# Performance work log

Measured on AMD Instinct MI355X. Metric: run time of the kernel, lower is better.

Reference implementation:

```python
import jax, jax.numpy as jnp
import numpy as np

N = 50000      # nodes
E = 800000     # edges (avg degree 16)
D = 96         # input_size == output_size
C = 10         # n_class
STEPS = 4      # num_layers -> GGNN propagation steps


def setup_inputs() -> dict:
    key = jax.random.key(0)
    ks = jax.random.split(key, 12)
    s = 1.0 / np.sqrt(D)
    return {
        "x": jax.random.normal(ks[0], (N, D), dtype=jnp.float32),
        "src": jax.random.randint(ks[1], (E,), 0, N, dtype=jnp.int32),
        "dst": jax.random.randint(ks[2], (E,), 0, N, dtype=jnp.int32),
        # edge message transform (DGL GatedGraphConv: Linear(out, out) per etype, 1 etype)
        "W_e": jax.random.normal(ks[3], (D, D), dtype=jnp.float32) * s,
        "b_e": jax.random.normal(ks[4], (D,), dtype=jnp.float32) * s,
        # GRUCell params (torch layout: rows ordered r, z, n)
        "W_ih": jax.random.normal(ks[5], (3 * D, D), dtype=jnp.float32) * s,
        "W_hh": jax.random.normal(ks[6], (3 * D, D), dtype=jnp.float32) * s,
        "b_ih": jax.random.normal(ks[7], (3 * D,), dtype=jnp.float32) * s,
        "b_hh": jax.random.normal(ks[8], (3 * D,), dtype=jnp.float32) * s,
        # classifier head
        "W_fc": jax.random.normal(ks[9], (C, D), dtype=jnp.float32) * s,
        "b_fc": jax.random.normal(ks[10], (C,), dtype=jnp.float32) * s,
    }


def _gru_cell(a, h, W_ih, W_hh, b_ih, b_hh):
    # torch.nn.GRUCell math; gate order r, z, n
    gx = a @ W_ih.T + b_ih            # [N, 3D]
    gh = h @ W_hh.T + b_hh            # [N, 3D]
    xr, xz, xn = jnp.split(gx, 3, axis=-1)
    hr, hz, hn = jnp.split(gh, 3, axis=-1)
    r = jax.nn.sigmoid(xr + hr)
    z = jax.nn.sigmoid(xz + hz)
    n = jnp.tanh(xn + r * hn)
    return (1.0 - z) * n + z * h


def reference(x, src, dst, W_e, b_e, W_ih, W_hh, b_ih, b_hh, W_fc, b_fc):
    h = x  # in_feats == out_feats, no padding needed
    for _ in range(STEPS):
        m = h @ W_e.T + b_e                                  # per-node transform [N, D]
        a = jax.ops.segment_sum(m[src], dst, num_segments=N) # gather + scatter-add [N, D]
        h = _gru_cell(a, h, W_ih, W_hh, b_ih, b_hh)
    logits = jax.nn.elu(h) @ W_fc.T + b_fc                   # [N, C]
    return logits
```

## Files before the change

### kernel.cpp

```cpp
#include <hip/hip_runtime.h>

static constexpr int D = 96;
static constexpr int G3 = 3 * D;
static constexpr int NSTEPS = 4;
static constexpr int NT = 18;
static constexpr int SCAN_BLK = 1024;
static constexpr int SLP = 104;
static constexpr int PLS = 97;
static constexpr int PLANE = 16 * PLS;

typedef __attribute__((ext_vector_type(8))) _Float16 f16x8;
typedef __attribute__((ext_vector_type(4))) _Float16 f16x4;
typedef __attribute__((ext_vector_type(4))) float f32x4;

__device__ __forceinline__ f16x8 load_a_frag(const _Float16* __restrict__ base,
                                             int r0, int lane, int kc) {
  int row = r0 + (lane & 15);
  int k0 = kc * 32 + ((lane >> 4) << 3);
  return *(const f16x8*)(base + (size_t)row * D + k0);
}

__device__ __forceinline__ f16x8 load_b_swz(const _Float16* __restrict__ W,
                                            int t, int kc, int lane) {
  return *(const f16x8*)(W + (((size_t)t * 3 + kc) * 64 + lane) * 8);
}


__global__ void convert_x_kernel(const float* __restrict__ x,
                                 _Float16* __restrict__ h, int total4) {
  int i = blockIdx.x * blockDim.x + threadIdx.x;
  if (i >= total4) return;
  float4 v = ((const float4*)x)[i];
  f16x4 o;
  o[0] = (_Float16)v.x; o[1] = (_Float16)v.y;
  o[2] = (_Float16)v.z; o[3] = (_Float16)v.w;
  *(f16x4*)(h + (size_t)i * 4) = o;
}

__global__ void compute_wx_kernel(const float* __restrict__ Wih,
                                  const float* __restrict__ We,
                                  const float* __restrict__ be,
                                  float* __restrict__ Wx,
                                  float* __restrict__ bxe) {
  int idx = blockIdx.x * blockDim.x + threadIdx.x;
  if (idx < G3 * D) {
    int r = idx / D, k = idx - r * D;
    float acc = 0.f;
    for (int c = 0; c < D; ++c) acc += Wih[r * D + c] * We[c * D + k];
    Wx[idx] = acc;
  } else if (idx < G3 * D + G3) {
    int r = idx - G3 * D;
    float acc = 0.f;
    for (int c = 0; c < D; ++c) acc += Wih[r * D + c] * be[c];
    bxe[r] = acc;
  }
}

__global__ void swizzle_f16_kernel(const float* __restrict__ Wx,
                                   const float* __restrict__ Whh,
                                   _Float16* __restrict__ WxF,
                                   _Float16* __restrict__ WhhF) {
  int idx = blockIdx.x * blockDim.x + threadIdx.x;
  if (idx >= 2 * NT * 3 * 64) return;
  int mat = idx / (NT * 3 * 64);
  int rem = idx - mat * (NT * 3 * 64);
  int t = rem / (3 * 64);
  int rem2 = rem - t * (3 * 64);
  int kc = rem2 >> 6;
  int lane = rem2 & 63;
  int c = t * 16 + (lane & 15);
  int k0 = kc * 32 + ((lane >> 4) << 3);
  const float* W = mat ? Whh : Wx;
  _Float16* dF = mat ? WhhF : WxF;
  f16x8 o;
#pragma unroll
  for (int j = 0; j < 8; ++j) o[j] = (_Float16)W[(size_t)c * D + k0 + j];
  *(f16x8*)(dF + (((size_t)t * 3 + kc) * 64 + lane) * 8) = o;
}


__global__ void hist_kernel(const int* __restrict__ dst, int* __restrict__ counts, int E) {
  int e = blockIdx.x * blockDim.x + threadIdx.x;
  if (e < E) atomicAdd(&counts[dst[e]], 1);
}

__global__ void partial_sum_kernel(const int* __restrict__ counts,
                                   int* __restrict__ blk_sums, int n) {
  __shared__ int red[256];
  int base = blockIdx.x * SCAN_BLK;
  int tid = threadIdx.x;
  int s = 0;
#pragma unroll
  for (int j = 0; j < 4; ++j) {
    int i = base + j * 256 + tid;
    if (i < n) s += counts[i];
  }
  red[tid] = s;
  __syncthreads();
  for (int off = 128; off > 0; off >>= 1) {
    if (tid < off) red[tid] += red[tid + off];
    __syncthreads();
  }
  if (tid == 0) blk_sums[blockIdx.x] = red[0];
}

__global__ void scan_offsets_kernel(const int* __restrict__ blk_sums,
                                    int* __restrict__ blk_off,
                                    int* __restrict__ row_ptr, int nb, int n) {
  __shared__ int lds[64];
  int tid = threadIdx.x;
  if (tid < nb) lds[tid] = blk_sums[tid];
  __syncthreads();
  if (tid == 0) {
    int run = 0;
    for (int i = 0; i < nb; ++i) { blk_off[i] = run; run += lds[i]; }
    row_ptr[n] = run;
  }
}

__global__ void block_scan_kernel(const int* __restrict__ counts,
                                  const int* __restrict__ blk_off,
                                  int* __restrict__ row_ptr, int n) {
  __shared__ int red[256];
  int base = blockIdx.x * SCAN_BLK;
  int tid = threadIdx.x;
  int i0 = base + tid * 4;
  int v0 = 0, v1 = 0, v2 = 0, v3 = 0;
  if (i0 + 3 < n) {
    int4 c = *(const int4*)(counts + i0);
    v0 = c.x; v1 = c.y; v2 = c.z; v3 = c.w;
  } else {
    if (i0 < n) v0 = counts[i0];
    if (i0 + 1 < n) v1 = counts[i0 + 1];
    if (i0 + 2 < n) v2 = counts[i0 + 2];
  }
  int tsum = v0 + v1 + v2 + v3;
  red[tid] = tsum;
  __syncthreads();
  for (int off = 1; off < 256; off <<= 1) {
    int t = (tid >= off) ? red[tid - off] : 0;
    __syncthreads();
    red[tid] += t;
    __syncthreads();
  }
  int excl = blk_off[blockIdx.x] + red[tid] - tsum;
  if (i0 < n) row_ptr[i0] = excl;
  if (i0 + 1 < n) row_ptr[i0 + 1] = excl + v0;
  if (i0 + 2 < n) row_ptr[i0 + 2] = excl + v0 + v1;
  if (i0 + 3 < n) row_ptr[i0 + 3] = excl + v0 + v1 + v2;
}

__global__ void route_kernel(const int* __restrict__ src, const int* __restrict__ dst,
                             const int* __restrict__ row_ptr,
                             int* __restrict__ bucket_fill,
                             unsigned* __restrict__ stage, int E, int n) {
  __shared__ int cnt[64], gbase[64], rpb[64];
  int tid = threadIdx.x;
  int base = blockIdx.x * 1024;
  if (tid < 64) {
    cnt[tid] = 0;
    int node = tid << 10;
    rpb[tid] = row_ptr[node < n ? node : n];
  }
  __syncthreads();
  int b[4], lp[4], sv[4], dl[4];
#pragma unroll
  for (int j = 0; j < 4; ++j) {
    int e = base + tid * 4 + j;
    if (e < E) {
      sv[j] = src[e];
      int d = dst[e];
      b[j] = d >> 10;
      dl[j] = d & 1023;
      lp[j] = atomicAdd(&cnt[b[j]], 1);
    } else {
      b[j] = -1;
    }
  }
  __syncthreads();
  if (tid < 64) {
    int c = cnt[tid];
    gbase[tid] = (c > 0) ? atomicAdd(&bucket_fill[tid], c) : 0;
  }
  __syncthreads();
#pragma unroll
  for (int j = 0; j < 4; ++j) {
    if (b[j] >= 0) {
      int pos = rpb[b[j]] + gbase[b[j]] + lp[j];
      stage[pos] = (unsigned)sv[j] | ((unsigned)dl[j] << 16);
    }
  }
}

__global__ void local_fill_kernel(const unsigned* __restrict__ stage,
                                  const int* __restrict__ row_ptr,
                                  unsigned short* __restrict__ csr_src, int n) {
  __shared__ int rp[1024];
  __shared__ int lf[1024];
  int b = blockIdx.x;
  int node0 = b << 10;
  int nn = n - node0; if (nn > 1024) nn = 1024;
  int tid = threadIdx.x;
  if (tid < nn) { rp[tid] = row_ptr[node0 + tid]; lf[tid] = 0; }
  __syncthreads();
  int ebeg = row_ptr[node0];
  int eend = row_ptr[node0 + nn];
  for (int i = ebeg + tid; i < eend; i += 1024) {
    unsigned p = stage[i];
    int dl = p >> 16;
    int s = p & 0xFFFF;
    int pos = rp[dl] + atomicAdd(&lf[dl], 1);
    csr_src[pos] = (unsigned short)s;
  }
}


__device__ __forceinline__ void gru_epilogue(const float* lds,
                                             const _Float16* __restrict__ h,
                                             _Float16* __restrict__ hout,
                                             const int* __restrict__ row_ptr,
                                             const float* __restrict__ bxe,
                                             const float* __restrict__ bih,
                                             const float* __restrict__ bhh,
                                             int base_row, int tid) {
#pragma unroll
  for (int j = 0; j < 4; ++j) {
    int e = tid + j * 384;
    int row = e / D;
    int col = e - row * D;
    int grow = base_row + row;
    int a = row * PLS + col;
    float degf = (float)(row_ptr[grow + 1] - row_ptr[grow]);
    float R  = lds[a] + lds[PLANE + a];
    float Z  = lds[2 * PLANE + a] + lds[3 * PLANE + a];
    float XN = lds[4 * PLANE + a];
    float HN = lds[5 * PLANE + a];
    float rg = 1.0f / (1.0f + __expf(-(R + bih[col] + bhh[col] + degf * bxe[col])));
    float zg = 1.0f / (1.0f + __expf(-(Z + bih[D + col] + bhh[D + col] + degf * bxe[D + col])));
    float ng = tanhf(XN + bih[2 * D + col] + degf * bxe[2 * D + col] + rg * (HN + bhh[2 * D + col]));
    float hv = (float)h[(size_t)grow * D + col];
    hout[(size_t)grow * D + col] = (_Float16)((1.0f - zg) * ng + zg * hv);
  }
}

__global__ __launch_bounds__(384) void gru_fused_kernel(
    const _Float16* __restrict__ h, _Float16* __restrict__ hout,
    const int* __restrict__ row_ptr, const unsigned short* __restrict__ csr_src,
    const _Float16* __restrict__ WxF, const _Float16* __restrict__ WhhF,
    const float* __restrict__ bxe, const float* __restrict__ bih,
    const float* __restrict__ bhh, int n) {
  __shared__ float lds[6 * PLANE];
  _Float16* sl = (_Float16*)&lds[4 * PLANE];
  int r0 = blockIdx.x << 5;
  int tid = threadIdx.x;
  int w = tid >> 6;
  int lane = tid & 63;

  {
    int row = tid / 12;
    int part = tid - row * 12;
    int grow = r0 + row;
    float acc[8];
#pragma unroll
    for (int j = 0; j < 8; ++j) acc[j] = 0.f;
    if (grow < n) {
      int beg = row_ptr[grow], end = row_ptr[grow + 1];
      const _Float16* hp = h + (size_t)part * 8;
      int e = beg;
      for (; e + 7 < end; e += 8) {
        f16x8 v0 = *(const f16x8*)(hp + (size_t)csr_src[e] * D);
        f16x8 v1 = *(const f16x8*)(hp + (size_t)csr_src[e + 1] * D);
        f16x8 v2 = *(const f16x8*)(hp + (size_t)csr_src[e + 2] * D);
        f16x8 v3 = *(const f16x8*)(hp + (size_t)csr_src[e + 3] * D);
        f16x8 v4 = *(const f16x8*)(hp + (size_t)csr_src[e + 4] * D);
        f16x8 v5 = *(const f16x8*)(hp + (size_t)csr_src[e + 5] * D);
        f16x8 v6 = *(const f16x8*)(hp + (size_t)csr_src[e + 6] * D);
        f16x8 v7 = *(const f16x8*)(hp + (size_t)csr_src[e + 7] * D);
#pragma unroll
        for (int j = 0; j < 8; ++j)
          acc[j] += (((float)v0[j] + (float)v1[j]) + ((float)v2[j] + (float)v3[j])) +
                    (((float)v4[j] + (float)v5[j]) + ((float)v6[j] + (float)v7[j]));
      }
      if (e + 3 < end) {
        f16x8 v0 = *(const f16x8*)(hp + (size_t)csr_src[e] * D);
        f16x8 v1 = *(const f16x8*)(hp + (size_t)csr_src[e + 1] * D);
        f16x8 v2 = *(const f16x8*)(hp + (size_t)csr_src[e + 2] * D);
        f16x8 v3 = *(const f16x8*)(hp + (size_t)csr_src[e + 3] * D);
#pragma unroll
        for (int j = 0; j < 8; ++j)
          acc[j] += ((float)v0[j] + (float)v1[j]) + ((float)v2[j] + (float)v3[j]);
        e += 4;
      }
      for (; e < end; ++e) {
        f16x8 v = *(const f16x8*)(hp + (size_t)csr_src[e] * D);
#pragma unroll
        for (int j = 0; j < 8; ++j) acc[j] += (float)v[j];
      }
    }
    f16x8 o;
#pragma unroll
    for (int j = 0; j < 8; ++j) o[j] = (_Float16)acc[j];
    *(f16x8*)&sl[row * SLP + part * 8] = o;
  }
  __syncthreads();

  const int opS = (w < 3) ? 1 : 0;
  const _Float16* WF = opS ? WxF : WhhF;
  const int wg = opS ? w : (w - 3);
  const int t0 = wg * 6;
  const int plane = wg * 2 + (opS ? 0 : 1);

  f16x8 a0[3], a1[3];
  if (opS) {
#pragma unroll
    for (int kc = 0; kc < 3; ++kc) {
      int k0 = kc * 32 + ((lane >> 4) << 3);
      a0[kc] = *(const f16x8*)&sl[(lane & 15) * SLP + k0];
      a1[kc] = *(const f16x8*)&sl[(16 + (lane & 15)) * SLP + k0];
    }
  } else {
#pragma unroll
    for (int kc = 0; kc < 3; ++kc) {
      a0[kc] = load_a_frag(h, r0, lane, kc);
      a1[kc] = load_a_frag(h, r0 + 16, lane, kc);
    }
  }
  __syncthreads();

  f32x4 acc0[6], acc1[6];
#pragma unroll
  for (int t = 0; t < 6; ++t) {
    acc0[t] = (f32x4){0.f, 0.f, 0.f, 0.f};
    acc1[t] = (f32x4){0.f, 0.f, 0.f, 0.f};
  }

#pragma unroll
  for (int ct = 0; ct < 6; ++ct)
#pragma unroll
    for (int kc = 0; kc < 3; ++kc) {
      f16x8 b = load_b_swz(WF, t0 + ct, kc, lane);
      acc0[ct] = __builtin_amdgcn_mfma_f32_16x16x32_f16(a0[kc], b, acc0[ct], 0, 0, 0);
      acc1[ct] = __builtin_amdgcn_mfma_f32_16x16x32_f16(a1[kc], b, acc1[ct], 0, 0, 0);
    }

  int col_l = lane & 15;
  int rq = (lane >> 4) << 2;
#pragma unroll
  for (int ct = 0; ct < 6; ++ct)
#pragma unroll
    for (int q = 0; q < 4; ++q)
      lds[plane * PLANE + (rq + q) * PLS + ct * 16 + col_l] = acc0[ct][q];
  __syncthreads();
  gru_epilogue(lds, h, hout, row_ptr, bxe, bih, bhh, r0, tid);
  __syncthreads();
  if (r0 + 16 < n) {
#pragma unroll
    for (int ct = 0; ct < 6; ++ct)
#pragma unroll
      for (int q = 0; q < 4; ++q)
        lds[plane * PLANE + (rq + q) * PLS + ct * 16 + col_l] = acc1[ct][q];
    __syncthreads();
    gru_epilogue(lds, h, hout, row_ptr, bxe, bih, bhh, r0 + 16, tid);
  }
}

__global__ void head_kernel(const _Float16* __restrict__ h,
                            const float* __restrict__ Wfc,
                            const float* __restrict__ bfc,
                            float* __restrict__ out,
                            int n, int C) {
  int idx = blockIdx.x * blockDim.x + threadIdx.x;
  if (idx >= n * C) return;
  int i = idx / C;
  int c = idx - i * C;
  const _Float16* hr = h + (size_t)i * D;
  const float* wr = Wfc + (size_t)c * D;
  float acc = bfc[c];
#pragma unroll 8
  for (int k = 0; k < D; ++k) {
    float hv = (float)hr[k];
    float e = hv > 0.0f ? hv : (__expf(hv) - 1.0f);
    acc += e * wr[k];
  }
  out[idx] = acc;
}

extern "C" void kernel_launch(void* const* d_in, const int* in_sizes, int n_in,
                              void* d_out, int out_size, void* d_ws, size_t ws_size,
                              hipStream_t stream) {
  const float* x    = (const float*)d_in[0];
  const int*   src  = (const int*)d_in[1];
  const int*   dst  = (const int*)d_in[2];
  const float* W_e  = (const float*)d_in[3];
  const float* b_e  = (const float*)d_in[4];
  const float* W_ih = (const float*)d_in[5];
  const float* W_hh = (const float*)d_in[6];
  const float* b_ih = (const float*)d_in[7];
  const float* b_hh = (const float*)d_in[8];
  const float* W_fc = (const float*)d_in[9];
  const float* b_fc = (const float*)d_in[10];

  const int n = in_sizes[0] / D;
  const int E = in_sizes[1];
  const int C = out_size / n;

  _Float16* hA = (_Float16*)d_ws;
  _Float16* hB = hA + (size_t)n * D;
  float* Wx    = (float*)(hB + (size_t)n * D);
  _Float16* WxF  = (_Float16*)(Wx + (size_t)G3 * D);
  _Float16* WhhF = WxF + (size_t)G3 * D;
  float* bxe   = (float*)(WhhF + (size_t)G3 * D);
  int* counts  = (int*)(bxe + G3);
  int* bucket_fill = counts + n;
  int* row_ptr = bucket_fill + n;
  unsigned short* csr_src = (unsigned short*)(row_ptr + (n + 1));
  int* blk_sums = (int*)(csr_src + E);
  int* blk_off  = blk_sums + 64;
  unsigned* stage = (unsigned*)(blk_off + 64);

  const int threads = 256;
  const int nb = (n + SCAN_BLK - 1) / SCAN_BLK;
  const int NB = (n + 1023) >> 10;

  (void)hipMemsetAsync(counts, 0, (size_t)2 * n * sizeof(int), stream);
  hist_kernel<<<(E + threads - 1) / threads, threads, 0, stream>>>(dst, counts, E);
  partial_sum_kernel<<<nb, 256, 0, stream>>>(counts, blk_sums, n);
  scan_offsets_kernel<<<1, 64, 0, stream>>>(blk_sums, blk_off, row_ptr, nb, n);
  block_scan_kernel<<<nb, 256, 0, stream>>>(counts, blk_off, row_ptr, n);
  route_kernel<<<(E + 1023) / 1024, 256, 0, stream>>>(src, dst, row_ptr,
                                                      bucket_fill, stage, E, n);
  local_fill_kernel<<<NB, 1024, 0, stream>>>(stage, row_ptr, csr_src, n);
  compute_wx_kernel<<<(G3 * D + G3 + threads - 1) / threads, threads, 0, stream>>>(
      W_ih, W_e, b_e, Wx, bxe);
  swizzle_f16_kernel<<<(2 * NT * 3 * 64 + threads - 1) / threads, threads, 0, stream>>>(
      Wx, W_hh, WxF, WhhF);
  convert_x_kernel<<<((n * D / 4) + threads - 1) / threads, threads, 0, stream>>>(
      x, hA, n * D / 4);

  const int gridG = (n + 31) / 32;

  const _Float16* hcur = hA;
  _Float16* hnext = hB;
  for (int step = 0; step < NSTEPS; ++step) {
    gru_fused_kernel<<<gridG, 384, 0, stream>>>(hcur, hnext, row_ptr, csr_src,
                                                WxF, WhhF, bxe, b_ih, b_hh, n);
    const _Float16* t = hcur; hcur = hnext; hnext = (_Float16*)t;
  }

  const int gridH = (n * C + threads - 1) / threads;
  head_kernel<<<gridH, threads, 0, stream>>>(hcur, W_fc, b_fc, (float*)d_out, n, C);
}
```

Baseline: 342.2 us.

## Fuse weight prep kernels, fold x conversion into routing, sort CSR neighbors

Merges the Wx product and fp16 swizzle into one prep kernel that writes the swizzled fp16 weights directly, which drops the fp32 Wx intermediate and one launch. The x-to-fp16 conversion moves into route_kernel as a grid-stride loop, removing another launch. local_fill_kernel now insertion-sorts each node's source list so the gathers in the GRU kernel touch memory in a more ordered pattern. The per-node sort is serial per thread and adds preprocessing cost in exchange for better gather locality.

```diff
diff --git a/kernel.cpp b/kernel.cpp
--- a/kernel.cpp
+++ b/kernel.cpp
@@ -26,56 +26,49 @@
 }
 
 
-__global__ void convert_x_kernel(const float* __restrict__ x,
-                                 _Float16* __restrict__ h, int total4) {
-  int i = blockIdx.x * blockDim.x + threadIdx.x;
-  if (i >= total4) return;
-  float4 v = ((const float4*)x)[i];
-  f16x4 o;
-  o[0] = (_Float16)v.x; o[1] = (_Float16)v.y;
-  o[2] = (_Float16)v.z; o[3] = (_Float16)v.w;
-  *(f16x4*)(h + (size_t)i * 4) = o;
-}
-
-__global__ void compute_wx_kernel(const float* __restrict__ Wih,
-                                  const float* __restrict__ We,
-                                  const float* __restrict__ be,
-                                  float* __restrict__ Wx,
-                                  float* __restrict__ bxe) {
+__global__ void prep_weights_kernel(const float* __restrict__ Wih,
+                                    const float* __restrict__ Whh,
+                                    const float* __restrict__ We,
+                                    const float* __restrict__ be,
+                                    _Float16* __restrict__ WxF,
+                                    _Float16* __restrict__ WhhF,
+                                    float* __restrict__ bxe) {
   int idx = blockIdx.x * blockDim.x + threadIdx.x;
-  if (idx < G3 * D) {
-    int r = idx / D, k = idx - r * D;
+  const int SWZ = 2 * NT * 3 * 64;
+  if (idx < SWZ) {
+    int mat = idx / (NT * 3 * 64);
+    int rem = idx - mat * (NT * 3 * 64);
+    int t = rem / (3 * 64);
+    int rem2 = rem - t * (3 * 64);
+    int kc = rem2 >> 6;
+    int lane = rem2 & 63;
+    int c = t * 16 + (lane & 15);
+    int k0 = kc * 32 + ((lane >> 4) << 3);
+    f16x8 o;
+    if (mat == 0) {
+      float a[8] = {0.f, 0.f, 0.f, 0.f, 0.f, 0.f, 0.f, 0.f};
+      const float* wr = Wih + (size_t)c * D;
+      for (int c2 = 0; c2 < D; ++c2) {
+        float wv = wr[c2];
+        const float* werow = We + (size_t)c2 * D + k0;
+#pragma unroll
+        for (int j = 0; j < 8; ++j) a[j] += wv * werow[j];
+      }
+#pragma unroll
+      for (int j = 0; j < 8; ++j) o[j] = (_Float16)a[j];
+      *(f16x8*)(WxF + (((size_t)t * 3 + kc) * 64 + lane) * 8) = o;
+    } else {
+#pragma unroll
+      for (int j = 0; j < 8; ++j) o[j] = (_Float16)Whh[(size_t)c * D + k0 + j];
+      *(f16x8*)(WhhF + (((size_t)t * 3 + kc) * 64 + lane) * 8) = o;
+    }
+  } else if (idx < SWZ + G3) {
+    int r = idx - SWZ;
     float acc = 0.f;
-    for (int c = 0; c < D; ++c) acc += Wih[r * D + c] * We[c * D + k];
-    Wx[idx] = acc;
-  } else if (idx < G3 * D + G3) {
-    int r = idx - G3 * D;
-    float acc = 0.f;
-    for (int c = 0; c < D; ++c) acc += Wih[r * D + c] * be[c];
+    const float* wr = Wih + (size_t)r * D;
+    for (int c = 0; c < D; ++c) acc += wr[c] * be[c];
     bxe[r] = acc;
   }
-}
-
-__global__ void swizzle_f16_kernel(const float* __restrict__ Wx,
-                                   const float* __restrict__ Whh,
-                                   _Float16* __restrict__ WxF,
-                                   _Float16* __restrict__ WhhF) {
-  int idx = blockIdx.x * blockDim.x + threadIdx.x;
-  if (idx >= 2 * NT * 3 * 64) return;
-  int mat = idx / (NT * 3 * 64);
-  int rem = idx - mat * (NT * 3 * 64);
-  int t = rem / (3 * 64);
-  int rem2 = rem - t * (3 * 64);
-  int kc = rem2 >> 6;
-  int lane = rem2 & 63;
-  int c = t * 16 + (lane & 15);
-  int k0 = kc * 32 + ((lane >> 4) << 3);
-  const float* W = mat ? Whh : Wx;
-  _Float16* dF = mat ? WhhF : WxF;
-  f16x8 o;
-#pragma unroll
-  for (int j = 0; j < 8; ++j) o[j] = (_Float16)W[(size_t)c * D + k0 + j];
-  *(f16x8*)(dF + (((size_t)t * 3 + kc) * 64 + lane) * 8) = o;
 }
 
 
@@ -153,7 +146,9 @@
 __global__ void route_kernel(const int* __restrict__ src, const int* __restrict__ dst,
                              const int* __restrict__ row_ptr,
                              int* __restrict__ bucket_fill,
-                             unsigned* __restrict__ stage, int E, int n) {
+                             unsigned* __restrict__ stage, int E, int n,
+                             const float* __restrict__ x,
+                             _Float16* __restrict__ hA, int total4) {
   __shared__ int cnt[64], gbase[64], rpb[64];
   int tid = threadIdx.x;
   int base = blockIdx.x * 1024;
@@ -190,6 +185,14 @@
       stage[pos] = (unsigned)sv[j] | ((unsigned)dl[j] << 16);
     }
   }
+  for (int i = blockIdx.x * blockDim.x + threadIdx.x; i < total4;
+       i += gridDim.x * blockDim.x) {
+    float4 v = ((const float4*)x)[i];
+    f16x4 o;
+    o[0] = (_Float16)v.x; o[1] = (_Float16)v.y;
+    o[2] = (_Float16)v.z; o[3] = (_Float16)v.w;
+    *(f16x4*)(hA + (size_t)i * 4) = o;
+  }
 }
 
 __global__ void local_fill_kernel(const unsigned* __restrict__ stage,
@@ -211,6 +214,17 @@
     int s = p & 0xFFFF;
     int pos = rp[dl] + atomicAdd(&lf[dl], 1);
     csr_src[pos] = (unsigned short)s;
+  }
+  __syncthreads();
+  if (tid < nn) {
+    int b0 = rp[tid];
+    int e0 = (tid + 1 < nn) ? rp[tid + 1] : eend;
+    for (int i = b0 + 1; i < e0; ++i) {
+      unsigned short key = csr_src[i];
+      int j = i - 1;
+      while (j >= b0 && csr_src[j] > key) { csr_src[j + 1] = csr_src[j]; --j; }
+      csr_src[j + 1] = key;
+    }
   }
 }
 
@@ -406,8 +420,7 @@
 
   _Float16* hA = (_Float16*)d_ws;
   _Float16* hB = hA + (size_t)n * D;
-  float* Wx    = (float*)(hB + (size_t)n * D);
-  _Float16* WxF  = (_Float16*)(Wx + (size_t)G3 * D);
+  _Float16* WxF  = hB + (size_t)n * D;
   _Float16* WhhF = WxF + (size_t)G3 * D;
   float* bxe   = (float*)(WhhF + (size_t)G3 * D);
   int* counts  = (int*)(bxe + G3);
@@ -421,6 +434,7 @@
   const int threads = 256;
   const int nb = (n + SCAN_BLK - 1) / SCAN_BLK;
   const int NB = (n + 1023) >> 10;
+  const int total4 = n * D / 4;
 
   (void)hipMemsetAsync(counts, 0, (size_t)2 * n * sizeof(int), stream);
   hist_kernel<<<(E + threads - 1) / threads, threads, 0, stream>>>(dst, counts, E);
@@ -428,14 +442,11 @@
   scan_offsets_kernel<<<1, 64, 0, stream>>>(blk_sums, blk_off, row_ptr, nb, n);
   block_scan_kernel<<<nb, 256, 0, stream>>>(counts, blk_off, row_ptr, n);
   route_kernel<<<(E + 1023) / 1024, 256, 0, stream>>>(src, dst, row_ptr,
-                                                      bucket_fill, stage, E, n);
+                                                      bucket_fill, stage, E, n,
+                                                      x, hA, total4);
   local_fill_kernel<<<NB, 1024, 0, stream>>>(stage, row_ptr, csr_src, n);
-  compute_wx_kernel<<<(G3 * D + G3 + threads - 1) / threads, threads, 0, stream>>>(
-      W_ih, W_e, b_e, Wx, bxe);
-  swizzle_f16_kernel<<<(2 * NT * 3 * 64 + threads - 1) / threads, threads, 0, stream>>>(
-      Wx, W_hh, WxF, WhhF);
-  convert_x_kernel<<<((n * D / 4) + threads - 1) / threads, threads, 0, stream>>>(
-      x, hA, n * D / 4);
+  prep_weights_kernel<<<(2 * NT * 3 * 64 + G3 + threads - 1) / threads, threads, 0,
+                        stream>>>(W_ih, W_hh, W_e, b_e, WxF, WhhF, bxe);
 
   const int gridG = (n + 31) / 32;
 
```

New measurement: 437.2 us. 27.8% more time.
